# Kernel tuning notes

Measured on AMD Instinct MI355X. Metric: run time of the kernel, lower is better.

## Reference

```python
import jax, jax.numpy as jnp
import numpy as np

TEMPERATURE = 0.1
EPS = 1e-12  # matches torch F.normalize default eps

def setup_inputs() -> dict:
    key = jax.random.key(0)
    k1, k2 = jax.random.split(key)
    z1 = jax.random.normal(k1, (2, 64, 64, 64), dtype=jnp.float32)  # (b, d, h, w)
    z2 = jax.random.normal(k2, (2, 64, 64, 64), dtype=jnp.float32)
    return {"z1": z1, "z2": z2}

def _flatten_normalize(z):
    b, d, h, w = z.shape
    z = jnp.transpose(z, (0, 2, 3, 1)).reshape(-1, d)  # (N, d), N = b*h*w
    norm = jnp.maximum(jnp.linalg.norm(z, axis=1, keepdims=True), EPS)
    return z / norm

def reference(z1, z2):
    z1n = _flatten_normalize(z1)  # (N, d)
    z2n = _flatten_normalize(z2)  # (N, d)
    sim = jnp.matmul(z1n, z2n.T) / TEMPERATURE  # (N, N)
    # cross-entropy with labels = arange(N): mean(logsumexp(row) - diag)
    lse = jax.nn.logsumexp(sim, axis=1)
    diag = jnp.diagonal(sim)
    return jnp.mean(lse - diag)
```

## Files before the change

kernel.cpp:

```cpp
#include <hip/hip_runtime.h>
#include <math.h>

#define N_PIX 8192
#define D 64
#define HW 4096
#define BSTRIDE 262144
#define C1 14.4269504088896340736f
#define LN2 0.6931471805599453f
#define NSEG 32
#define SEGCOLS 256
#define BC 256

typedef __attribute__((ext_vector_type(8))) short short8;
typedef __attribute__((ext_vector_type(4))) float f32x4;

#define LDS_AS __attribute__((address_space(3)))
#define GLB_AS __attribute__((address_space(1)))

__device__ inline ushort f2bf(float x) {
    uint u = __float_as_uint(x);
    return (ushort)((u + 0x7FFFu + ((u >> 16) & 1u)) >> 16);
}
__device__ inline float bflo(uint u) { return __uint_as_float(u << 16); }
__device__ inline float bfhi(uint u) { return __uint_as_float(u & 0xFFFF0000u); }

__device__ inline void gll16(const ushort* g, ushort* l) {
    __builtin_amdgcn_global_load_lds((const GLB_AS uint*)g, (LDS_AS uint*)l, 16, 0, 0);
}

__device__ inline void stage(const ushort* __restrict__ z2b, int jcol,
                             ushort* ldsbuf, int wave, int lane) {
    int l3 = lane >> 3, l7 = lane & 7;
    int xo = (l7 ^ l3) << 3;
#pragma unroll
    for (int q = 0; q < BC / 32; ++q) {
        int c = wave * (BC / 32) + q;
        const ushort* src = z2b + (size_t)(jcol + c * 8 + l3) * D + xo;
        gll16(src, ldsbuf + c * 512);
    }
}

__global__ __launch_bounds__(256) void knorm(const float* __restrict__ z1,
                                             const float* __restrict__ z2,
                                             ushort* __restrict__ z1b,
                                             ushort* __restrict__ z2b,
                                             float* __restrict__ out) {
    int gid = blockIdx.x * 256 + threadIdx.x;
    if (gid == 0) out[0] = 0.f;
    int q = gid & 7;
    int pixg = gid >> 3;
    int t = pixg >> 13;
    int n = pixg & (N_PIX - 1);
    const float* src = t ? z2 : z1;
    ushort* dst = t ? z2b : z1b;
    int b = n >> 12;
    int p = n & 4095;
    const float* base = src + b * BSTRIDE + (q * 8) * HW + p;
    float v[8];
    float ss = 0.f;
#pragma unroll
    for (int c = 0; c < 8; ++c) { v[c] = base[(size_t)c * HW]; ss = fmaf(v[c], v[c], ss); }
    ss += __shfl_xor(ss, 1);
    ss += __shfl_xor(ss, 2);
    ss += __shfl_xor(ss, 4);
    float inv = 1.0f / fmaxf(sqrtf(ss), 1e-12f);
    float sc = t ? inv : inv * C1;
    uint4 w;
#pragma unroll
    for (int j = 0; j < 4; ++j) {
        ((uint*)&w)[j] = (uint)f2bf(v[2 * j] * sc) | ((uint)f2bf(v[2 * j + 1] * sc) << 16);
    }
    *(uint4*)(dst + (size_t)n * D + q * 8) = w;
}

__global__ __launch_bounds__(256, 4) void ksim(const ushort* __restrict__ z1b,
                                               const ushort* __restrict__ z2b,
                                               float* __restrict__ ps) {
    __shared__ ushort lds[BC * D];
    int tid = threadIdx.x;
    int wave = tid >> 6, lane = tid & 63;
    int lrow = lane & 15;
    int lk = lane >> 4;
    int rbase = blockIdx.x * 256 + wave * 64;
    int jbase = blockIdx.y * SEGCOLS;

    stage(z2b, jbase, lds, wave, lane);

    const ushort* ar = z1b + (size_t)(rbase + lrow) * D + lk * 8;
    short8 a0[4], a1[4];
#pragma unroll
    for (int rt = 0; rt < 4; ++rt) {
        a0[rt] = *(const short8*)(ar + rt * 16 * D);
        a1[rt] = *(const short8*)(ar + rt * 16 * D + 32);
    }

    float s[16];
#pragma unroll
    for (int i = 0; i < 16; ++i) s[i] = 0.f;

    __syncthreads();

    const char* bb = (const char*)lds;
    int sw = (lrow & 7);
    f32x4 z = {0.f, 0.f, 0.f, 0.f};

#pragma unroll
    for (int ct = 0; ct < BC / 16; ++ct) {
        int rowoff = (ct * 16 + lrow) << 7;
        short8 blo = *(const short8*)(bb + rowoff + ((lk ^ sw) << 4));
        short8 bhi = *(const short8*)(bb + rowoff + (((4 + lk) ^ sw) << 4));
#pragma unroll
        for (int rt = 0; rt < 4; ++rt) {
            f32x4 acc = __builtin_amdgcn_mfma_f32_16x16x32_bf16(a0[rt], blo, z, 0, 0, 0);
            acc = __builtin_amdgcn_mfma_f32_16x16x32_bf16(a1[rt], bhi, acc, 0, 0, 0);
#pragma unroll
            for (int r = 0; r < 4; ++r)
                s[rt * 4 + r] += __builtin_amdgcn_exp2f(acc[r]);
        }
    }

#pragma unroll
    for (int off = 1; off <= 8; off <<= 1) {
#pragma unroll
        for (int i = 0; i < 16; ++i) s[i] += __shfl_xor(s[i], off);
    }
    if (lrow == 0) {
        int seg = blockIdx.y;
#pragma unroll
        for (int rt = 0; rt < 4; ++rt)
#pragma unroll
            for (int r = 0; r < 4; ++r)
                ps[(size_t)(rbase + rt * 16 + lk * 4 + r) * NSEG + seg] = s[rt * 4 + r];
    }
}

__global__ __launch_bounds__(64) void kfinal(const ushort* __restrict__ z1b,
                                             const ushort* __restrict__ z2b,
                                             const float* __restrict__ ps,
                                             float* __restrict__ out) {
    int tid = threadIdx.x;
    int row = blockIdx.x * 64 + tid;

    const f32x4* pp = (const f32x4*)(ps + (size_t)row * NSEG);
    float s = 0.f;
#pragma unroll
    for (int q = 0; q < NSEG / 4; ++q) {
        f32x4 v = pp[q];
        s += (v[0] + v[1]) + (v[2] + v[3]);
    }
    const uint4* xp = (const uint4*)(z1b + (size_t)row * D);
    const uint4* yp = (const uint4*)(z2b + (size_t)row * D);
    float d = 0.f;
#pragma unroll
    for (int q = 0; q < 8; ++q) {
        uint4 x = xp[q], y = yp[q];
        d = fmaf(bflo(x.x), bflo(y.x), d); d = fmaf(bfhi(x.x), bfhi(y.x), d);
        d = fmaf(bflo(x.y), bflo(y.y), d); d = fmaf(bfhi(x.y), bfhi(y.y), d);
        d = fmaf(bflo(x.z), bflo(y.z), d); d = fmaf(bfhi(x.z), bfhi(y.z), d);
        d = fmaf(bflo(x.w), bflo(y.w), d); d = fmaf(bfhi(x.w), bfhi(y.w), d);
    }
    float val = __logf(s) - LN2 * d;

#pragma unroll
    for (int off = 32; off > 0; off >>= 1) val += __shfl_down(val, off);
    if (tid == 0) atomicAdd(out, val * (1.0f / (float)N_PIX));
}

extern "C" void kernel_launch(void* const* d_in, const int* in_sizes, int n_in,
                              void* d_out, int out_size, void* d_ws, size_t ws_size,
                              hipStream_t stream) {
    const float* z1 = (const float*)d_in[0];
    const float* z2 = (const float*)d_in[1];
    float* out = (float*)d_out;

    ushort* z1b = (ushort*)d_ws;
    ushort* z2b = z1b + (size_t)N_PIX * D;
    float* ps   = (float*)(z2b + (size_t)N_PIX * D);

    knorm<<<512, 256, 0, stream>>>(z1, z2, z1b, z2b, out);
    dim3 g2(N_PIX / 256, NSEG);
    ksim<<<g2, 256, 0, stream>>>(z1b, z2b, ps);
    kfinal<<<N_PIX / 64, 64, 0, stream>>>(z1b, z2b, ps, out);
}
```

Measured before the change: 26.70 us.

## Halve rows per block and double-buffer MFMA accumulators to overlap exp with matmul

Each wave of the similarity kernel now covers 32 rows instead of 64, so the grid doubles to 64x32 blocks. The column-tile loop is software-pipelined with two accumulator banks: the MFMAs for the next 16-column tile are issued while the exp2 sums for the previous tile are computed. The aim is to hide MFMA latency behind transcendental work and to raise the number of blocks in flight. The cost is twice as many blocks, each staging the same 256-column LDS tile of z2, so total LDS traffic and global loads of z2 double.

```diff
diff --git a/kernel.cpp b/kernel.cpp
--- a/kernel.cpp
+++ b/kernel.cpp
@@ -81,53 +81,72 @@
     int wave = tid >> 6, lane = tid & 63;
     int lrow = lane & 15;
     int lk = lane >> 4;
-    int rbase = blockIdx.x * 256 + wave * 64;
+    int rbase = blockIdx.x * 128 + wave * 32;
     int jbase = blockIdx.y * SEGCOLS;
 
     stage(z2b, jbase, lds, wave, lane);
 
     const ushort* ar = z1b + (size_t)(rbase + lrow) * D + lk * 8;
-    short8 a0[4], a1[4];
-#pragma unroll
-    for (int rt = 0; rt < 4; ++rt) {
+    short8 a0[2], a1[2];
+#pragma unroll
+    for (int rt = 0; rt < 2; ++rt) {
         a0[rt] = *(const short8*)(ar + rt * 16 * D);
         a1[rt] = *(const short8*)(ar + rt * 16 * D + 32);
     }
 
-    float s[16];
-#pragma unroll
-    for (int i = 0; i < 16; ++i) s[i] = 0.f;
+    float s[8];
+#pragma unroll
+    for (int i = 0; i < 8; ++i) s[i] = 0.f;
 
     __syncthreads();
 
     const char* bb = (const char*)lds;
     int sw = (lrow & 7);
     f32x4 z = {0.f, 0.f, 0.f, 0.f};
-
-#pragma unroll
-    for (int ct = 0; ct < BC / 16; ++ct) {
-        int rowoff = (ct * 16 + lrow) << 7;
-        short8 blo = *(const short8*)(bb + rowoff + ((lk ^ sw) << 4));
-        short8 bhi = *(const short8*)(bb + rowoff + (((4 + lk) ^ sw) << 4));
-#pragma unroll
-        for (int rt = 0; rt < 4; ++rt) {
-            f32x4 acc = __builtin_amdgcn_mfma_f32_16x16x32_bf16(a0[rt], blo, z, 0, 0, 0);
-            acc = __builtin_amdgcn_mfma_f32_16x16x32_bf16(a1[rt], bhi, acc, 0, 0, 0);
-#pragma unroll
-            for (int r = 0; r < 4; ++r)
-                s[rt * 4 + r] += __builtin_amdgcn_exp2f(acc[r]);
-        }
-    }
+    f32x4 accA[2], accB[2];
+
+#define ACCBLK(BANK, CT)                                                            \
+    {                                                                               \
+        int rowoff = ((CT) * 16 + lrow) << 7;                                       \
+        short8 blo = *(const short8*)(bb + rowoff + ((lk ^ sw) << 4));              \
+        short8 bhi = *(const short8*)(bb + rowoff + (((4 + lk) ^ sw) << 4));        \
+        _Pragma("unroll")                                                           \
+        for (int rt = 0; rt < 2; ++rt) {                                            \
+            f32x4 t0 = __builtin_amdgcn_mfma_f32_16x16x32_bf16(a0[rt], blo, z, 0, 0, 0); \
+            BANK[rt] = __builtin_amdgcn_mfma_f32_16x16x32_bf16(a1[rt], bhi, t0, 0, 0, 0); \
+        }                                                                           \
+    }
+#define EXPBLK(BANK)                                                                \
+    _Pragma("unroll")                                                               \
+    for (int rt = 0; rt < 2; ++rt) {                                                \
+        _Pragma("unroll")                                                           \
+        for (int r = 0; r < 4; ++r)                                                 \
+            s[rt * 4 + r] += __builtin_amdgcn_exp2f(BANK[rt][r]);                   \
+    }
+
+    ACCBLK(accA, 0)
+#pragma unroll
+    for (int c2 = 0; c2 < 7; ++c2) {
+        ACCBLK(accB, 2 * c2 + 1)
+        EXPBLK(accA)
+        ACCBLK(accA, 2 * c2 + 2)
+        EXPBLK(accB)
+    }
+    ACCBLK(accB, 15)
+    EXPBLK(accA)
+    EXPBLK(accB)
+#undef ACCBLK
+#undef EXPBLK
 
 #pragma unroll
     for (int off = 1; off <= 8; off <<= 1) {
 #pragma unroll
-        for (int i = 0; i < 16; ++i) s[i] += __shfl_xor(s[i], off);
+        for (int i = 0; i < 8; ++i) s[i] += __shfl_xor(s[i], off);
     }
     if (lrow == 0) {
         int seg = blockIdx.y;
 #pragma unroll
-        for (int rt = 0; rt < 4; ++rt)
+        for (int rt = 0; rt < 2; ++rt)
 #pragma unroll
             for (int r = 0; r < 4; ++r)
                 ps[(size_t)(rbase + rt * 16 + lk * 4 + r) * NSEG + seg] = s[rt * 4 + r];
@@ -178,7 +197,7 @@
     float* ps   = (float*)(z2b + (size_t)N_PIX * D);
 
     knorm<<<512, 256, 0, stream>>>(z1, z2, z1b, z2b, out);
-    dim3 g2(N_PIX / 256, NSEG);
+    dim3 g2(N_PIX / 128, NSEG);
     ksim<<<g2, 256, 0, stream>>>(z1b, z2b, ps);
     kfinal<<<N_PIX / 64, 64, 0, stream>>>(z1b, z2b, ps, out);
 }
```

New measurement: 26.69 us, median of 2. No clear change (-0.0%).
